# Kernel tuning notes

Measured on AMD Instinct MI355X. Metric: run time of the kernel, lower is better.

Reference implementation:

```python
import jax, jax.numpy as jnp
import numpy as np
from jax.ops import segment_sum

N = 100000
E = 1600000
IN_C = 128
WIDTHS = [128, 64, 32, 16, 8]  # hidden_feats=128 -> /1,/2,/4,/8,/16


def setup_inputs() -> dict:
    key = jax.random.key(0)
    ks = jax.random.split(key, 12)
    x = jax.random.normal(ks[0], (N, IN_C), dtype=jnp.float32)
    edge_index = jax.random.randint(ks[1], (2, E), 0, N, dtype=jnp.int64)
    inp = {"x": x, "edge_index": edge_index}
    fan_in = [IN_C] + WIDTHS[:-1]
    for i, (fi, fo) in enumerate(zip(fan_in, WIDTHS)):
        # Glorot init like PyG GCNConv
        lim = float(np.sqrt(6.0 / (fi + fo)))
        inp[f"W{i+1}"] = jax.random.uniform(ks[2 + i], (fi, fo), dtype=jnp.float32, minval=-lim, maxval=lim)
        inp[f"b{i+1}"] = jnp.zeros((fo,), dtype=jnp.float32)
    return inp


def _gcn_norm(edge_index):
    # add self loops, compute D^{-1/2} (A+I) D^{-1/2} edge weights
    loops = jnp.arange(N, dtype=edge_index.dtype)
    src = jnp.concatenate([edge_index[0], loops])  # [E+N]
    dst = jnp.concatenate([edge_index[1], loops])
    deg = segment_sum(jnp.ones_like(dst, dtype=jnp.float32), dst, num_segments=N)
    dinv = jnp.where(deg > 0, jax.lax.rsqrt(jnp.maximum(deg, 1.0)), 0.0)
    norm = dinv[src] * dinv[dst]  # [E+N]
    return src, dst, norm


def _gcn_layer(x, W, b, src, dst, norm):
    h = x @ W                         # [N, Fout] linear transform first (PyG order)
    msg = h[src] * norm[:, None]      # gather + edge scaling, [E+N, Fout]
    out = segment_sum(msg, dst, num_segments=N)  # scatter-add aggregation
    return out + b


def reference(x, edge_index, W1, b1, W2, b2, W3, b3, W4, b4, W5, b5):
    src, dst, norm = _gcn_norm(edge_index)
    params = [(W1, b1), (W2, b2), (W3, b3), (W4, b4), (W5, b5)]
    h = x
    for W, b in params:
        h = jax.nn.relu(_gcn_layer(h, W, b, src, dst, norm))
    return h
```

## Files before the change

### kernel.cpp

```cpp
#include <hip/hip_runtime.h>
#include <hip/hip_bf16.h>
#include <hip/hip_fp16.h>


#define LDSE16  2048
#define LDSE16B 3072
#define LDSE8H  6144
#define PCHUNK 4096
#define BNODES 512
#define MAXBUK 256

typedef float floatx4 __attribute__((ext_vector_type(4)));
typedef _Float16 f16x4 __attribute__((ext_vector_type(4)));
typedef _Float16 f16x8 __attribute__((ext_vector_type(8)));

__global__ __launch_bounds__(256) void k_bucket(const int* __restrict__ src,
                                                const int* __restrict__ dst,
                                                int2* __restrict__ pairs,
                                                int* __restrict__ bcnt,
                                                int E, int nbk, int CAP) {
    __shared__ int  hist[MAXBUK], pre[MAXBUK], cur[MAXBUK], gbase[MAXBUK], tmp[MAXBUK];
    __shared__ int2 arena[PCHUNK];
    const int tid = threadIdx.x;
    const int e0  = blockIdx.x * PCHUNK;
    const int m   = (E - e0 < PCHUNK) ? (E - e0) : PCHUNK;

    hist[tid] = 0;
    __syncthreads();

    int dl[PCHUNK / 256], sl[PCHUNK / 256], rl[PCHUNK / 256];
#pragma unroll
    for (int j = 0; j < PCHUNK / 256; ++j) {
        int i = j * 256 + tid;
        rl[j] = -1;
        if (i < m) {
            dl[j] = __builtin_nontemporal_load(&dst[e0 + i]);
            sl[j] = __builtin_nontemporal_load(&src[e0 + i]);
            rl[j] = dl[j] >> 9;
            atomicAdd(&hist[rl[j]], 1);
        }
    }
    __syncthreads();
    int v = hist[tid];
    tmp[tid] = v;
    __syncthreads();
    for (int off = 1; off < MAXBUK; off <<= 1) {
        int t = (tid >= off) ? tmp[tid - off] : 0;
        __syncthreads();
        tmp[tid] += t;
        __syncthreads();
    }
    pre[tid] = tmp[tid] - v;
    cur[tid] = 0;
    __syncthreads();
#pragma unroll
    for (int j = 0; j < PCHUNK / 256; ++j) {
        if (rl[j] >= 0) {
            int slot = pre[rl[j]] + atomicAdd(&cur[rl[j]], 1);
            arena[slot] = make_int2(dl[j], sl[j]);
        }
    }
    __syncthreads();
    if (tid < nbk && hist[tid] > 0) gbase[tid] = atomicAdd(&bcnt[tid], hist[tid]);
    __syncthreads();
    const int wave = tid >> 6, lane = tid & 63;
    for (int r = wave; r < nbk; r += 4) {
        int cnt = hist[r];
        if (cnt == 0) continue;
        int b0 = pre[r], g = gbase[r];
        for (int j = lane; j < cnt; j += 64)
            pairs[(size_t)r * CAP + g + j] = arena[b0 + j];
    }
}

__global__ __launch_bounds__(256) void k_sortfill(const int2* __restrict__ pairs,
                                                  const int* __restrict__ bcnt,
                                                  int* __restrict__ csr_src,
                                                  int* __restrict__ offsets,
                                                  float* __restrict__ dinv,
                                                  int n, int E, int nbk, int CAP) {
    __shared__ int hist[BNODES], lofs[BNODES], cur[BNODES], tmp[256];
    __shared__ int sbase;
    const int r    = blockIdx.x;
    const int tid  = threadIdx.x;
    const int node0 = r * BNODES;
    const int2* p = pairs + (size_t)r * CAP;

    int bv = (tid < nbk) ? bcnt[tid] : 0;
    tmp[tid] = bv;
    __syncthreads();
    for (int off = 1; off < 256; off <<= 1) {
        int t = (tid >= off) ? tmp[tid - off] : 0;
        __syncthreads();
        tmp[tid] += t;
        __syncthreads();
    }
    if (tid == r) sbase = tmp[r] - bv;
    if (r == nbk - 1 && tid == 0) offsets[n] = E;
    __syncthreads();
    const int m    = bcnt[r];
    const int base = sbase;

    for (int l = tid; l < BNODES; l += 256) hist[l] = 0;
    __syncthreads();
    for (int i = tid; i < m; i += 256)
        atomicAdd(&hist[p[i].x - node0], 1);
    __syncthreads();
    int a = hist[2 * tid], b = hist[2 * tid + 1];
    int s = a + b;
    tmp[tid] = s;
    __syncthreads();
    for (int off = 1; off < 256; off <<= 1) {
        int t = (tid >= off) ? tmp[tid - off] : 0;
        __syncthreads();
        tmp[tid] += t;
        __syncthreads();
    }
    int exc = tmp[tid] - s;
    lofs[2 * tid]     = exc;
    lofs[2 * tid + 1] = exc + a;
    cur[2 * tid] = 0;
    cur[2 * tid + 1] = 0;
    __syncthreads();
    for (int i = tid; i < m; i += 256) {
        int2 e = p[i];
        int l = e.x - node0;
        int pos = lofs[l] + atomicAdd(&cur[l], 1);
        csr_src[base + pos] = e.y;
    }
    for (int l = tid; l < BNODES; l += 256) {
        int node = node0 + l;
        if (node < n) {
            offsets[node] = base + lofs[l];
            dinv[node]    = rsqrtf((float)(hist[l] + 1));
        }
    }
}

template <int FIN, int FOUT, bool H16IN>
__global__ __launch_bounds__(512) void k_mgemm(const float* __restrict__ x,
                                               const float* __restrict__ W,
                                               const float* __restrict__ dinv,
                                               _Float16* __restrict__ g, int n) {
    constexpr int KC  = (FIN < 64) ? FIN : 64;
    constexpr int NKQ = KC / 4;
    constexpr int AP  = KC + 8;
    constexpr int NT  = FOUT / 16;
    __shared__ _Float16 As[128 * AP];
    __shared__ _Float16 Ws[FOUT * AP];
    __shared__ float dv[128];

    const int tid  = threadIdx.x;
    const int wave = tid >> 6;
    const int lane = tid & 63;
    const int m0   = blockIdx.x * 128;

    if (tid < 128) dv[tid] = (m0 + tid < n) ? dinv[m0 + tid] : 0.f;

    floatx4 acc[NT];
#pragma unroll
    for (int t = 0; t < NT; ++t) acc[t] = (floatx4)(0.f);

    for (int kc0 = 0; kc0 < FIN; kc0 += KC) {
        __syncthreads();
        if constexpr (H16IN) {
            const _Float16* xh = reinterpret_cast<const _Float16*>(x);
            constexpr int NC8 = KC / 8;
            for (int s = tid; s < 128 * NC8; s += 512) {
                int node = s / NC8, c8 = s % NC8;
                int gn = m0 + node, f0 = kc0 + c8 * 8;
                f16x8 h = (f16x8)(_Float16)0;
                if (gn < n)
                    h = *reinterpret_cast<const f16x8*>(
                        &xh[((size_t)(f0 >> 5) * n + gn) * 32 + (f0 & 31)]);
                *reinterpret_cast<f16x8*>(&As[node * AP + c8 * 8]) = h;
            }
        } else {
            const floatx4* x4 = reinterpret_cast<const floatx4*>(x);
            for (int s = tid; s < 128 * NKQ; s += 512) {
                int node = s / NKQ, kq = s % NKQ;
                int gn = m0 + node, gslot = kc0 / 4 + kq;
                floatx4 v = (floatx4)(0.f);
                if (gn < n)
                    v = __builtin_nontemporal_load(&x4[(size_t)gn * (FIN / 4) + gslot]);
                f16x4 h = {(_Float16)v.x, (_Float16)v.y, (_Float16)v.z, (_Float16)v.w};
                *reinterpret_cast<f16x4*>(&As[node * AP + kq * 4]) = h;
            }
        }
        for (int s = tid; s < FOUT * NKQ; s += 512) {
            int fo = s % FOUT, kq = s / FOUT;
            int k = kc0 + kq * 4;
            f16x4 h = {(_Float16)W[(k + 0) * FOUT + fo], (_Float16)W[(k + 1) * FOUT + fo],
                       (_Float16)W[(k + 2) * FOUT + fo], (_Float16)W[(k + 3) * FOUT + fo]};
            *reinterpret_cast<f16x4*>(&Ws[fo * AP + kq * 4]) = h;
        }
        __syncthreads();
#pragma unroll
        for (int kk = 0; kk < KC / 32; ++kk) {
            const int ka = kk * 32 + ((lane >> 4) << 2);
            const _Float16* ap = &As[(wave * 16 + (lane & 15)) * AP + ka];
            f16x4 alo = *reinterpret_cast<const f16x4*>(ap);
            f16x4 ahi = *reinterpret_cast<const f16x4*>(ap + 16);
            f16x8 a = {alo[0], alo[1], alo[2], alo[3], ahi[0], ahi[1], ahi[2], ahi[3]};
#pragma unroll
            for (int t = 0; t < NT; ++t) {
                const _Float16* bp = &Ws[(t * 16 + (lane & 15)) * AP + ka];
                f16x4 blo = *reinterpret_cast<const f16x4*>(bp);
                f16x4 bhi = *reinterpret_cast<const f16x4*>(bp + 16);
                f16x8 b = {blo[0], blo[1], blo[2], blo[3], bhi[0], bhi[1], bhi[2], bhi[3]};
                acc[t] = __builtin_amdgcn_mfma_f32_16x16x32_f16(a, b, acc[t], 0, 0, 0);
            }
        }
    }

    const int i0 = (lane >> 4) << 2;
#pragma unroll
    for (int r = 0; r < 4; ++r) {
        int nl = wave * 16 + i0 + r;
        int node = m0 + nl;
        if (node < n) {
            float d = dv[nl];
#pragma unroll
            for (int t = 0; t < NT; ++t) {
                int fo = t * 16 + (lane & 15);
                g[((size_t)(fo >> 5) * n + node) * 32 + (fo & 31)] = (_Float16)(acc[t][r] * d);
            }
        }
    }
}

template <int FIN, int FOUT, int NR, int NC>
__global__ __launch_bounds__(256) void k_gemm(const _Float16* __restrict__ xh,
                                              const float* __restrict__ W,
                                              const float* __restrict__ dinv,
                                              _Float16* __restrict__ gh, int n) {
    constexpr int NFG = FOUT / NC;
    constexpr int M   = NR * (256 / NFG);
    constexpr int KC  = (FIN < 32) ? FIN : 32;
    constexpr int MP  = M + 4;
    constexpr int WP  = KC * NC + 4;
    __shared__ float Wl[NFG * WP];
    __shared__ float xt[KC * MP];

    const int tid = threadIdx.x;
    const int fg  = tid % NFG;
    const int mg  = tid / NFG;
    const int m0  = blockIdx.x * M;

    float acc[NR][NC];
#pragma unroll
    for (int i = 0; i < NR; ++i)
#pragma unroll
        for (int j = 0; j < NC; ++j) acc[i][j] = 0.f;

    for (int kc0 = 0; kc0 < FIN; kc0 += KC) {
        __syncthreads();
        for (int idx = tid; idx < KC * FOUT; idx += 256) {
            int k  = idx / FOUT;
            int fo = idx % FOUT;
            Wl[(fo / NC) * WP + k * NC + (fo % NC)] = W[(kc0 + k) * FOUT + fo];
        }
        constexpr int SL8 = KC / 8;
        for (int s = tid; s < M * SL8; s += 256) {
            int ml = s / SL8;
            int c8 = s % SL8;
            int gn = m0 + ml;
            f16x8 h = (f16x8)(_Float16)0;
            if (gn < n)
                h = *reinterpret_cast<const f16x8*>(&xh[(size_t)gn * FIN + kc0 + c8 * 8]);
#pragma unroll
            for (int j = 0; j < 8; ++j)
                xt[(c8 * 8 + j) * MP + ml] = (float)h[j];
        }
        __syncthreads();
#pragma unroll 4
        for (int k = 0; k < KC; ++k) {
            float xr[NR], wr[NC];
#pragma unroll
            for (int p = 0; p < NR / 4; ++p) {
                float4 v = *reinterpret_cast<const float4*>(&xt[k * MP + mg * NR + p * 4]);
                xr[p * 4 + 0] = v.x; xr[p * 4 + 1] = v.y;
                xr[p * 4 + 2] = v.z; xr[p * 4 + 3] = v.w;
            }
#pragma unroll
            for (int p = 0; p < NC / 4; ++p) {
                float4 v = *reinterpret_cast<const float4*>(&Wl[fg * WP + k * NC + p * 4]);
                wr[p * 4 + 0] = v.x; wr[p * 4 + 1] = v.y;
                wr[p * 4 + 2] = v.z; wr[p * 4 + 3] = v.w;
            }
#pragma unroll
            for (int i = 0; i < NR; ++i)
#pragma unroll
                for (int j = 0; j < NC; ++j) acc[i][j] += xr[i] * wr[j];
        }
    }

#pragma unroll
    for (int i = 0; i < NR; ++i) {
        int gn = m0 + mg * NR + i;
        if (gn < n) {
            float d = dinv[gn];
            f16x4 o;
#pragma unroll
            for (int j = 0; j < NC; ++j) o[j] = (_Float16)(acc[i][j] * d);
            *reinterpret_cast<f16x4*>(&gh[(size_t)gn * FOUT + fg * NC]) = o;
        }
    }
}

#define ACCUM8(A, v) {                                                        \
    union { float4 f; __half2 h[4]; } u_; u_.f = (v);                         \
    _Pragma("unroll")                                                         \
    for (int j_ = 0; j_ < 4; ++j_) {                                          \
        float2 f_ = __half22float2(u_.h[j_]);                                 \
        A[2 * j_] += f_.x; A[2 * j_ + 1] += f_.y;                             \
    } }

template <bool H16OUT>
__global__ __launch_bounds__(256) void k_aggrh(const float4* __restrict__ gh,
                                               const int* __restrict__ offsets,
                                               const int* __restrict__ csr_src,
                                               const float* __restrict__ dinv,
                                               const float* __restrict__ bias,
                                               float4* __restrict__ outb,
                                               int n, int nsl, int sl0) {
    __shared__ int eidx[LDSE16];
    const int sl     = sl0 + blockIdx.x % nsl;
    const int nb     = blockIdx.x / nsl;
    const int node0  = nb * 64;
    const int nodeHi = (node0 + 64 < n) ? node0 + 64 : n;
    const int node   = node0 + (threadIdx.x >> 2);
    const int q      = threadIdx.x & 3;

    const int eS = offsets[node0];
    const int eE = offsets[nodeHi];
    const int C  = eE - eS;
    const bool useLds = (C <= LDSE16);

    const bool alive = (node < n);
    int e0 = 0, e1 = 0;
    float dnode = 0.f;
    const float4* gs = gh + (size_t)sl * n * 4;
    float A[8], B[8];
#pragma unroll
    for (int j = 0; j < 8; ++j) { A[j] = 0.f; B[j] = 0.f; }
    if (alive) {
        e0 = offsets[node];
        e1 = offsets[node + 1];
        dnode = dinv[node];
        float4 vs = gs[(size_t)node * 4 + q];
        ACCUM8(A, vs);
    }

    if (useLds) {
        for (int i = threadIdx.x; i < C; i += 256)
            eidx[i] = __builtin_nontemporal_load(&csr_src[eS + i]);
    }
    __syncthreads();
    if (!alive) return;

    const int m = e1 - e0;
    int i = 0;
    if (useLds) {
        const int le = e0 - eS;
        for (; i + 8 <= m; i += 8) {
            int s0 = eidx[le + i + 0], s1 = eidx[le + i + 1];
            int s2 = eidx[le + i + 2], s3 = eidx[le + i + 3];
            int s4 = eidx[le + i + 4], s5 = eidx[le + i + 5];
            int s6 = eidx[le + i + 6], s7 = eidx[le + i + 7];
            float4 v0 = gs[(size_t)s0 * 4 + q], v1 = gs[(size_t)s1 * 4 + q];
            float4 v2 = gs[(size_t)s2 * 4 + q], v3 = gs[(size_t)s3 * 4 + q];
            float4 v4 = gs[(size_t)s4 * 4 + q], v5 = gs[(size_t)s5 * 4 + q];
            float4 v6 = gs[(size_t)s6 * 4 + q], v7 = gs[(size_t)s7 * 4 + q];
            ACCUM8(A, v0); ACCUM8(B, v1); ACCUM8(A, v2); ACCUM8(B, v3);
            ACCUM8(A, v4); ACCUM8(B, v5); ACCUM8(A, v6); ACCUM8(B, v7);
        }
        for (; i + 4 <= m; i += 4) {
            int s0 = eidx[le + i + 0], s1 = eidx[le + i + 1];
            int s2 = eidx[le + i + 2], s3 = eidx[le + i + 3];
            float4 v0 = gs[(size_t)s0 * 4 + q], v1 = gs[(size_t)s1 * 4 + q];
            float4 v2 = gs[(size_t)s2 * 4 + q], v3 = gs[(size_t)s3 * 4 + q];
            ACCUM8(A, v0); ACCUM8(B, v1); ACCUM8(A, v2); ACCUM8(B, v3);
        }
        for (; i < m; ++i) {
            float4 v = gs[(size_t)eidx[le + i] * 4 + q];
            ACCUM8(A, v);
        }
    } else {
        for (; i + 4 <= m; i += 4) {
            int s0 = csr_src[e0 + i + 0], s1 = csr_src[e0 + i + 1];
            int s2 = csr_src[e0 + i + 2], s3 = csr_src[e0 + i + 3];
            float4 v0 = gs[(size_t)s0 * 4 + q], v1 = gs[(size_t)s1 * 4 + q];
            float4 v2 = gs[(size_t)s2 * 4 + q], v3 = gs[(size_t)s3 * 4 + q];
            ACCUM8(A, v0); ACCUM8(B, v1); ACCUM8(A, v2); ACCUM8(B, v3);
        }
        for (; i < m; ++i) {
            float4 v = gs[(size_t)csr_src[e0 + i] * 4 + q];
            ACCUM8(A, v);
        }
    }

    const float* bf = bias + sl * 32 + q * 8;
    float r[8];
#pragma unroll
    for (int j = 0; j < 8; ++j)
        r[j] = fmaxf(dnode * (A[j] + B[j]) + bf[j], 0.f);

    if constexpr (H16OUT) {
        f16x8 o;
#pragma unroll
        for (int j = 0; j < 8; ++j) o[j] = (_Float16)r[j];
        _Float16* oh = reinterpret_cast<_Float16*>(outb);
        __builtin_nontemporal_store(
            o, reinterpret_cast<f16x8*>(&oh[((size_t)sl * n + node) * 32 + q * 8]));
    } else {
        floatx4 r0 = {r[0], r[1], r[2], r[3]};
        floatx4 r1 = {r[4], r[5], r[6], r[7]};
        floatx4* ob = reinterpret_cast<floatx4*>(outb);
        size_t base = ((size_t)(sl * 2 + (q >> 1)) * n + node) * 4 + (q & 1) * 2;
        __builtin_nontemporal_store(r0, &ob[base + 0]);
        __builtin_nontemporal_store(r1, &ob[base + 1]);
    }
}

__global__ __launch_bounds__(256) void k_aggr16h(const _Float16* __restrict__ gh,
                                                 const int* __restrict__ offsets,
                                                 const int* __restrict__ csr_src,
                                                 const float* __restrict__ dinv,
                                                 const float* __restrict__ bias,
                                                 _Float16* __restrict__ outh, int n) {
    __shared__ int eidx[LDSE16B];
    const int node0  = blockIdx.x * 128;
    const int nodeHi = (node0 + 128 < n) ? node0 + 128 : n;
    const int node   = node0 + (threadIdx.x >> 1);
    const int h      = threadIdx.x & 1;

    const int eS = offsets[node0];
    const int eE = offsets[nodeHi];
    const int C  = eE - eS;
    const bool useLds = (C <= LDSE16B);

    const bool alive = (node < n);
    int e0 = 0, e1 = 0;
    float dnode = 0.f;
    float A[8], B[8];
#pragma unroll
    for (int j = 0; j < 8; ++j) { A[j] = 0.f; B[j] = 0.f; }
    if (alive) {
        e0 = offsets[node];
        e1 = offsets[node + 1];
        dnode = dinv[node];
        f16x8 vs = *reinterpret_cast<const f16x8*>(&gh[(size_t)node * 16 + h * 8]);
#pragma unroll
        for (int j = 0; j < 8; ++j) A[j] += (float)vs[j];
    }

    if (useLds) {
        for (int i = threadIdx.x; i < C; i += 256)
            eidx[i] = __builtin_nontemporal_load(&csr_src[eS + i]);
    }
    __syncthreads();
    if (!alive) return;

    const int m = e1 - e0;
    int i = 0;
    if (useLds) {
        const int le = e0 - eS;
        for (; i + 4 <= m; i += 4) {
            int s0 = eidx[le + i + 0], s1 = eidx[le + i + 1];
            int s2 = eidx[le + i + 2], s3 = eidx[le + i + 3];
            f16x8 v0 = *reinterpret_cast<const f16x8*>(&gh[(size_t)s0 * 16 + h * 8]);
            f16x8 v1 = *reinterpret_cast<const f16x8*>(&gh[(size_t)s1 * 16 + h * 8]);
            f16x8 v2 = *reinterpret_cast<const f16x8*>(&gh[(size_t)s2 * 16 + h * 8]);
            f16x8 v3 = *reinterpret_cast<const f16x8*>(&gh[(size_t)s3 * 16 + h * 8]);
#pragma unroll
            for (int j = 0; j < 8; ++j) {
                A[j] += (float)v0[j] + (float)v2[j];
                B[j] += (float)v1[j] + (float)v3[j];
            }
        }
        for (; i < m; ++i) {
            f16x8 v = *reinterpret_cast<const f16x8*>(
                &gh[(size_t)eidx[le + i] * 16 + h * 8]);
#pragma unroll
            for (int j = 0; j < 8; ++j) A[j] += (float)v[j];
        }
    } else {
        for (; i < m; ++i) {
            f16x8 v = *reinterpret_cast<const f16x8*>(
                &gh[(size_t)csr_src[e0 + i] * 16 + h * 8]);
#pragma unroll
            for (int j = 0; j < 8; ++j) A[j] += (float)v[j];
        }
    }

    const float* bf = bias + h * 8;
    f16x8 o;
#pragma unroll
    for (int j = 0; j < 8; ++j)
        o[j] = (_Float16)fmaxf(dnode * (A[j] + B[j]) + bf[j], 0.f);
    __builtin_nontemporal_store(
        o, reinterpret_cast<f16x8*>(&outh[(size_t)node * 16 + h * 8]));
}

__global__ __launch_bounds__(256) void k_aggr8h(const _Float16* __restrict__ gh,
                                                const int* __restrict__ offsets,
                                                const int* __restrict__ csr_src,
                                                const float* __restrict__ dinv,
                                                const float* __restrict__ bias,
                                                float4* __restrict__ outb, int n) {
    __shared__ int eidx[LDSE8H];
    const int node0  = blockIdx.x * 256;
    const int nodeHi = (node0 + 256 < n) ? node0 + 256 : n;
    const int node   = node0 + threadIdx.x;

    const int eS = offsets[node0];
    const int eE = offsets[nodeHi];
    const int C  = eE - eS;
    const bool useLds = (C <= LDSE8H);

    const bool alive = (node < n);
    int e0 = 0, e1 = 0;
    float dnode = 0.f;
    float A[8], B[8];
#pragma unroll
    for (int j = 0; j < 8; ++j) { A[j] = 0.f; B[j] = 0.f; }
    if (alive) {
        e0 = offsets[node];
        e1 = offsets[node + 1];
        dnode = dinv[node];
        f16x8 vs = *reinterpret_cast<const f16x8*>(&gh[(size_t)node * 8]);
#pragma unroll
        for (int j = 0; j < 8; ++j) A[j] += (float)vs[j];
    }

    if (useLds) {
        for (int i = threadIdx.x; i < C; i += 256)
            eidx[i] = __builtin_nontemporal_load(&csr_src[eS + i]);
    }
    __syncthreads();
    if (!alive) return;

    const int m = e1 - e0;
    int i = 0;
    if (useLds) {
        const int le = e0 - eS;
        for (; i + 4 <= m; i += 4) {
            int s0 = eidx[le + i + 0], s1 = eidx[le + i + 1];
            int s2 = eidx[le + i + 2], s3 = eidx[le + i + 3];
            f16x8 v0 = *reinterpret_cast<const f16x8*>(&gh[(size_t)s0 * 8]);
            f16x8 v1 = *reinterpret_cast<const f16x8*>(&gh[(size_t)s1 * 8]);
            f16x8 v2 = *reinterpret_cast<const f16x8*>(&gh[(size_t)s2 * 8]);
            f16x8 v3 = *reinterpret_cast<const f16x8*>(&gh[(size_t)s3 * 8]);
#pragma unroll
            for (int j = 0; j < 8; ++j) {
                A[j] += (float)v0[j] + (float)v2[j];
                B[j] += (float)v1[j] + (float)v3[j];
            }
        }
        for (; i < m; ++i) {
            f16x8 v = *reinterpret_cast<const f16x8*>(&gh[(size_t)eidx[le + i] * 8]);
#pragma unroll
            for (int j = 0; j < 8; ++j) A[j] += (float)v[j];
        }
    } else {
        for (; i < m; ++i) {
            f16x8 v = *reinterpret_cast<const f16x8*>(&gh[(size_t)csr_src[e0 + i] * 8]);
#pragma unroll
            for (int j = 0; j < 8; ++j) A[j] += (float)v[j];
        }
    }

    floatx4 r0, r1;
    r0.x = fmaxf(dnode * (A[0] + B[0]) + bias[0], 0.f);
    r0.y = fmaxf(dnode * (A[1] + B[1]) + bias[1], 0.f);
    r0.z = fmaxf(dnode * (A[2] + B[2]) + bias[2], 0.f);
    r0.w = fmaxf(dnode * (A[3] + B[3]) + bias[3], 0.f);
    r1.x = fmaxf(dnode * (A[4] + B[4]) + bias[4], 0.f);
    r1.y = fmaxf(dnode * (A[5] + B[5]) + bias[5], 0.f);
    r1.z = fmaxf(dnode * (A[6] + B[6]) + bias[6], 0.f);
    r1.w = fmaxf(dnode * (A[7] + B[7]) + bias[7], 0.f);
    floatx4* ob = reinterpret_cast<floatx4*>(outb);
    __builtin_nontemporal_store(r0, &ob[(size_t)node * 2 + 0]);
    __builtin_nontemporal_store(r1, &ob[(size_t)node * 2 + 1]);
}

extern "C" void kernel_launch(void* const* d_in, const int* in_sizes, int n_in,
                              void* d_out, int out_size, void* d_ws, size_t ws_size,
                              hipStream_t stream) {
    const int N = in_sizes[0] / 128;
    const int E = in_sizes[1] / 2;
    const int nbk = (N + BNODES - 1) / BNODES;
    const int avg = (E + nbk - 1) / nbk;
    const int CAP = avg + avg / 4 + 512;

    const float* x   = (const float*)d_in[0];
    const int*   ei  = (const int*)d_in[1];
    const int*   src = ei;
    const int*   dst = ei + E;
    const float* W1 = (const float*)d_in[2],  *b1 = (const float*)d_in[3];
    const float* W2 = (const float*)d_in[4],  *b2 = (const float*)d_in[5];
    const float* W3 = (const float*)d_in[6],  *b3 = (const float*)d_in[7];
    const float* W4 = (const float*)d_in[8],  *b4 = (const float*)d_in[9];
    const float* W5 = (const float*)d_in[10], *b5 = (const float*)d_in[11];
    float* out = (float*)d_out;

    size_t off = 0;
    auto alloc = [&](size_t bytes) {
        void* p = (char*)d_ws + off;
        off += (bytes + 255) & ~(size_t)255;
        return p;
    };
    int*   offsets = (int*)alloc((size_t)(N + 1) * 4);
    float* dinv    = (float*)alloc((size_t)N * 4);
    int*   csr_src = (int*)alloc((size_t)E * 4);
    int*   bcnt    = (int*)alloc(MAXBUK * 4);
    int2*  pairs   = (int2*)alloc((size_t)nbk * CAP * 8);
    float* g       = (float*)alloc((size_t)N * 128 * 4);
    float* xbuf    = (float*)alloc((size_t)N * 128 * 4);

    (void)hipMemsetAsync(bcnt, 0, MAXBUK * 4, stream);

    const int TB = 256;
    int nb16  = (N + 63) / 64;
    int nb128 = (N + 127) / 128;
    int nb256 = (N + 255) / 256;
    int nch   = (E + PCHUNK - 1) / PCHUNK;

    k_bucket<<<nch, TB, 0, stream>>>(src, dst, pairs, bcnt, E, nbk, CAP);
    k_sortfill<<<nbk, TB, 0, stream>>>(pairs, bcnt, csr_src, offsets, dinv, N, E, nbk, CAP);

    const float4* g4  = (const float4*)g;
    float4*       xb4 = (float4*)xbuf;
    _Float16*     gh  = (_Float16*)g;
    _Float16*     xbh = (_Float16*)xbuf;

    k_mgemm<128, 128, false><<<nb128, 512, 0, stream>>>(x, W1, dinv, gh, N);
    k_aggrh<true><<<nb16 * 2, TB, 0, stream>>>(g4, offsets, csr_src, dinv, b1, xb4, N, 2, 0);
    k_aggrh<true><<<nb16 * 2, TB, 0, stream>>>(g4, offsets, csr_src, dinv, b1, xb4, N, 2, 2);
    k_mgemm<128, 64, true><<<nb128, 512, 0, stream>>>(xbuf, W2, dinv, gh, N);
    k_aggrh<true><<<nb16 * 2, TB, 0, stream>>>(g4, offsets, csr_src, dinv, b2, xb4, N, 2, 0);
    k_mgemm<64, 32, true><<<nb128, 512, 0, stream>>>(xbuf, W3, dinv, gh, N);
    k_aggrh<true><<<nb16 * 1, TB, 0, stream>>>(g4, offsets, csr_src, dinv, b3, xb4, N, 1, 0);
    k_gemm<32, 16, 4, 4><<<(N + 255) / 256, TB, 0, stream>>>(xbh, W4, dinv, gh, N);
    k_aggr16h<<<nb128, TB, 0, stream>>>(gh, offsets, csr_src, dinv, b4, xbh, N);
    k_gemm<16, 8, 4, 4><<<(N + 511) / 512, TB, 0, stream>>>(xbh, W5, dinv, gh, N);
    k_aggr8h<<<nb256, TB, 0, stream>>>(gh, offsets, csr_src, dinv, b5, (float4*)out, N);
}
```

Baseline: 378.0 us.

## Fuse small layer-4/5 GEMMs into preceding aggregation epilogues and merge layer-1 launches

Removes the standalone k_gemm kernels for the 32→16 and 16→8 transforms. Their matrix products now run in the epilogues of the layer-3 and layer-4 aggregation kernels. W is staged in LDS and the per-lane partial products are reduced with cross-lane shuffles, then scaled by dinv. This saves two kernel launches and a round trip of the intermediate activations through global memory. The two layer-1 aggregation launches are also merged into one grid covering all four slices. The cost is extra register pressure and FMA work in the aggregation epilogues.

```diff
diff --git a/kernel.cpp b/kernel.cpp
--- a/kernel.cpp
+++ b/kernel.cpp
@@ -229,85 +229,6 @@
     }
 }
 
-template <int FIN, int FOUT, int NR, int NC>
-__global__ __launch_bounds__(256) void k_gemm(const _Float16* __restrict__ xh,
-                                              const float* __restrict__ W,
-                                              const float* __restrict__ dinv,
-                                              _Float16* __restrict__ gh, int n) {
-    constexpr int NFG = FOUT / NC;
-    constexpr int M   = NR * (256 / NFG);
-    constexpr int KC  = (FIN < 32) ? FIN : 32;
-    constexpr int MP  = M + 4;
-    constexpr int WP  = KC * NC + 4;
-    __shared__ float Wl[NFG * WP];
-    __shared__ float xt[KC * MP];
-
-    const int tid = threadIdx.x;
-    const int fg  = tid % NFG;
-    const int mg  = tid / NFG;
-    const int m0  = blockIdx.x * M;
-
-    float acc[NR][NC];
-#pragma unroll
-    for (int i = 0; i < NR; ++i)
-#pragma unroll
-        for (int j = 0; j < NC; ++j) acc[i][j] = 0.f;
-
-    for (int kc0 = 0; kc0 < FIN; kc0 += KC) {
-        __syncthreads();
-        for (int idx = tid; idx < KC * FOUT; idx += 256) {
-            int k  = idx / FOUT;
-            int fo = idx % FOUT;
-            Wl[(fo / NC) * WP + k * NC + (fo % NC)] = W[(kc0 + k) * FOUT + fo];
-        }
-        constexpr int SL8 = KC / 8;
-        for (int s = tid; s < M * SL8; s += 256) {
-            int ml = s / SL8;
-            int c8 = s % SL8;
-            int gn = m0 + ml;
-            f16x8 h = (f16x8)(_Float16)0;
-            if (gn < n)
-                h = *reinterpret_cast<const f16x8*>(&xh[(size_t)gn * FIN + kc0 + c8 * 8]);
-#pragma unroll
-            for (int j = 0; j < 8; ++j)
-                xt[(c8 * 8 + j) * MP + ml] = (float)h[j];
-        }
-        __syncthreads();
-#pragma unroll 4
-        for (int k = 0; k < KC; ++k) {
-            float xr[NR], wr[NC];
-#pragma unroll
-            for (int p = 0; p < NR / 4; ++p) {
-                float4 v = *reinterpret_cast<const float4*>(&xt[k * MP + mg * NR + p * 4]);
-                xr[p * 4 + 0] = v.x; xr[p * 4 + 1] = v.y;
-                xr[p * 4 + 2] = v.z; xr[p * 4 + 3] = v.w;
-            }
-#pragma unroll
-            for (int p = 0; p < NC / 4; ++p) {
-                float4 v = *reinterpret_cast<const float4*>(&Wl[fg * WP + k * NC + p * 4]);
-                wr[p * 4 + 0] = v.x; wr[p * 4 + 1] = v.y;
-                wr[p * 4 + 2] = v.z; wr[p * 4 + 3] = v.w;
-            }
-#pragma unroll
-            for (int i = 0; i < NR; ++i)
-#pragma unroll
-                for (int j = 0; j < NC; ++j) acc[i][j] += xr[i] * wr[j];
-        }
-    }
-
-#pragma unroll
-    for (int i = 0; i < NR; ++i) {
-        int gn = m0 + mg * NR + i;
-        if (gn < n) {
-            float d = dinv[gn];
-            f16x4 o;
-#pragma unroll
-            for (int j = 0; j < NC; ++j) o[j] = (_Float16)(acc[i][j] * d);
-            *reinterpret_cast<f16x4*>(&gh[(size_t)gn * FOUT + fg * NC]) = o;
-        }
-    }
-}
-
 #define ACCUM8(A, v) {                                                        \
     union { float4 f; __half2 h[4]; } u_; u_.f = (v);                         \
     _Pragma("unroll")                                                         \
@@ -316,16 +237,18 @@
         A[2 * j_] += f_.x; A[2 * j_ + 1] += f_.y;                             \
     } }
 
-template <bool H16OUT>
+template <int FUSE>
 __global__ __launch_bounds__(256) void k_aggrh(const float4* __restrict__ gh,
                                                const int* __restrict__ offsets,
                                                const int* __restrict__ csr_src,
                                                const float* __restrict__ dinv,
                                                const float* __restrict__ bias,
-                                               float4* __restrict__ outb,
-                                               int n, int nsl, int sl0) {
+                                               const float* __restrict__ Wn,
+                                               _Float16* __restrict__ outh,
+                                               int n, int nsl) {
     __shared__ int eidx[LDSE16];
-    const int sl     = sl0 + blockIdx.x % nsl;
+    __shared__ float Wl[(FUSE > 0) ? 32 * FUSE : 1];
+    const int sl     = blockIdx.x % nsl;
     const int nb     = blockIdx.x / nsl;
     const int node0  = nb * 64;
     const int nodeHi = (node0 + 64 < n) ? node0 + 64 : n;
@@ -352,6 +275,9 @@
         ACCUM8(A, vs);
     }
 
+    if constexpr (FUSE > 0) {
+        for (int i = threadIdx.x; i < 32 * FUSE; i += 256) Wl[i] = Wn[i];
+    }
     if (useLds) {
         for (int i = threadIdx.x; i < C; i += 256)
             eidx[i] = __builtin_nontemporal_load(&csr_src[eS + i]);
@@ -406,20 +332,32 @@
     for (int j = 0; j < 8; ++j)
         r[j] = fmaxf(dnode * (A[j] + B[j]) + bf[j], 0.f);
 
-    if constexpr (H16OUT) {
+    if constexpr (FUSE == 16) {
+        float p[16];
+#pragma unroll
+        for (int f = 0; f < 16; ++f) p[f] = 0.f;
+#pragma unroll
+        for (int j = 0; j < 8; ++j) {
+            float rv = r[j];
+            const float* wr = &Wl[(q * 8 + j) * 16];
+#pragma unroll
+            for (int f = 0; f < 16; ++f) p[f] += rv * wr[f];
+        }
+#pragma unroll
+        for (int f = 0; f < 16; ++f) {
+            p[f] += __shfl_xor(p[f], 1);
+            p[f] += __shfl_xor(p[f], 2);
+        }
+        f16x4 o;
+#pragma unroll
+        for (int t = 0; t < 4; ++t) o[t] = (_Float16)(p[q * 4 + t] * dnode);
+        *reinterpret_cast<f16x4*>(&outh[(size_t)node * 16 + q * 4]) = o;
+    } else {
         f16x8 o;
 #pragma unroll
         for (int j = 0; j < 8; ++j) o[j] = (_Float16)r[j];
-        _Float16* oh = reinterpret_cast<_Float16*>(outb);
         __builtin_nontemporal_store(
-            o, reinterpret_cast<f16x8*>(&oh[((size_t)sl * n + node) * 32 + q * 8]));
-    } else {
-        floatx4 r0 = {r[0], r[1], r[2], r[3]};
-        floatx4 r1 = {r[4], r[5], r[6], r[7]};
-        floatx4* ob = reinterpret_cast<floatx4*>(outb);
-        size_t base = ((size_t)(sl * 2 + (q >> 1)) * n + node) * 4 + (q & 1) * 2;
-        __builtin_nontemporal_store(r0, &ob[base + 0]);
-        __builtin_nontemporal_store(r1, &ob[base + 1]);
+            o, reinterpret_cast<f16x8*>(&outh[((size_t)sl * n + node) * 32 + q * 8]));
     }
 }
 
@@ -428,8 +366,10 @@
                                                  const int* __restrict__ csr_src,
                                                  const float* __restrict__ dinv,
                                                  const float* __restrict__ bias,
+                                                 const float* __restrict__ Wn,
                                                  _Float16* __restrict__ outh, int n) {
     __shared__ int eidx[LDSE16B];
+    __shared__ float Wl[16 * 8];
     const int node0  = blockIdx.x * 128;
     const int nodeHi = (node0 + 128 < n) ? node0 + 128 : n;
     const int node   = node0 + (threadIdx.x >> 1);
@@ -455,6 +395,7 @@
         for (int j = 0; j < 8; ++j) A[j] += (float)vs[j];
     }
 
+    if (threadIdx.x < 128) Wl[threadIdx.x] = Wn[threadIdx.x];
     if (useLds) {
         for (int i = threadIdx.x; i < C; i += 256)
             eidx[i] = __builtin_nontemporal_load(&csr_src[eS + i]);
@@ -495,12 +436,27 @@
     }
 
     const float* bf = bias + h * 8;
-    f16x8 o;
+    float r[8];
 #pragma unroll
     for (int j = 0; j < 8; ++j)
-        o[j] = (_Float16)fmaxf(dnode * (A[j] + B[j]) + bf[j], 0.f);
-    __builtin_nontemporal_store(
-        o, reinterpret_cast<f16x8*>(&outh[(size_t)node * 16 + h * 8]));
+        r[j] = fmaxf(dnode * (A[j] + B[j]) + bf[j], 0.f);
+
+    float p[8];
+#pragma unroll
+    for (int f = 0; f < 8; ++f) p[f] = 0.f;
+#pragma unroll
+    for (int j = 0; j < 8; ++j) {
+        float rv = r[j];
+        const float* wr = &Wl[(h * 8 + j) * 8];
+#pragma unroll
+        for (int f = 0; f < 8; ++f) p[f] += rv * wr[f];
+    }
+#pragma unroll
+    for (int f = 0; f < 8; ++f) p[f] += __shfl_xor(p[f], 1);
+    f16x4 o;
+#pragma unroll
+    for (int t = 0; t < 4; ++t) o[t] = (_Float16)(p[h * 4 + t] * dnode);
+    *reinterpret_cast<f16x4*>(&outh[(size_t)node * 8 + h * 4]) = o;
 }
 
 __global__ __launch_bounds__(256) void k_aggr8h(const _Float16* __restrict__ gh,
@@ -631,19 +587,16 @@
     k_sortfill<<<nbk, TB, 0, stream>>>(pairs, bcnt, csr_src, offsets, dinv, N, E, nbk, CAP);
 
     const float4* g4  = (const float4*)g;
-    float4*       xb4 = (float4*)xbuf;
+    const float4* xb4 = (const float4*)xbuf;
     _Float16*     gh  = (_Float16*)g;
     _Float16*     xbh = (_Float16*)xbuf;
 
     k_mgemm<128, 128, false><<<nb128, 512, 0, stream>>>(x, W1, dinv, gh, N);
-    k_aggrh<true><<<nb16 * 2, TB, 0, stream>>>(g4, offsets, csr_src, dinv, b1, xb4, N, 2, 0);
-    k_aggrh<true><<<nb16 * 2, TB, 0, stream>>>(g4, offsets, csr_src, dinv, b1, xb4, N, 2, 2);
+    k_aggrh<0><<<nb16 * 4, TB, 0, stream>>>(g4, offsets, csr_src, dinv, b1, nullptr, xbh, N, 4);
     k_mgemm<128, 64, true><<<nb128, 512, 0, stream>>>(xbuf, W2, dinv, gh, N);
-    k_aggrh<true><<<nb16 * 2, TB, 0, stream>>>(g4, offsets, csr_src, dinv, b2, xb4, N, 2, 0);
+    k_aggrh<0><<<nb16 * 2, TB, 0, stream>>>(g4, offsets, csr_src, dinv, b2, nullptr, xbh, N, 2);
     k_mgemm<64, 32, true><<<nb128, 512, 0, stream>>>(xbuf, W3, dinv, gh, N);
-    k_aggrh<true><<<nb16 * 1, TB, 0, stream>>>(g4, offsets, csr_src, dinv, b3, xb4, N, 1, 0);
-    k_gemm<32, 16, 4, 4><<<(N + 255) / 256, TB, 0, stream>>>(xbh, W4, dinv, gh, N);
-    k_aggr16h<<<nb128, TB, 0, stream>>>(gh, offsets, csr_src, dinv, b4, xbh, N);
-    k_gemm<16, 8, 4, 4><<<(N + 511) / 512, TB, 0, stream>>>(xbh, W5, dinv, gh, N);
+    k_aggrh<16><<<nb16 * 1, TB, 0, stream>>>(g4, offsets, csr_src, dinv, b3, W4, xbh, N, 1);
+    k_aggr16h<<<nb128, TB, 0, stream>>>(xbh, offsets, csr_src, dinv, b4, W5, gh, N);
     k_aggr8h<<<nb256, TB, 0, stream>>>(gh, offsets, csr_src, dinv, b5, (float4*)out, N);
 }
```

Result: faster. 356.8 us (-5.6%).
